# Kernel tuning notes

Measured on AMD Instinct MI355X. Metric: run time of the kernel, lower is better.

## Reference

```python
import jax, jax.numpy as jnp
import numpy as np

N, E, F_IN, F_E, H, T = 100000, 1600000, 128, 16, 64, 32
NEG_SLOPE = 0.2


def setup_inputs() -> dict:
    key = jax.random.key(0)
    ks = jax.random.split(key, 24)
    s = 0.1
    inp = {
        'x': jax.random.normal(ks[0], (N, F_IN), jnp.float32),
        'edge_index': jax.random.randint(ks[1], (2, E), 0, N, dtype=jnp.int32),
        'edge_attr': jax.random.normal(ks[2], (E, F_E), jnp.float32),
        # GATConv layer 1 (heads=1)
        'W1': jax.random.normal(ks[3], (F_IN, H), jnp.float32) * s,
        'as1': jax.random.normal(ks[4], (H,), jnp.float32) * s,
        'ad1': jax.random.normal(ks[5], (H,), jnp.float32) * s,
        'We1': jax.random.normal(ks[6], (F_E, H), jnp.float32) * s,
        'ae1': jax.random.normal(ks[7], (H,), jnp.float32) * s,
        'b1': jnp.zeros((H,), jnp.float32),
        # GATConv layer 2
        'W2': jax.random.normal(ks[8], (H, H), jnp.float32) * s,
        'as2': jax.random.normal(ks[9], (H,), jnp.float32) * s,
        'ad2': jax.random.normal(ks[10], (H,), jnp.float32) * s,
        'We2': jax.random.normal(ks[11], (F_E, H), jnp.float32) * s,
        'ae2': jax.random.normal(ks[12], (H,), jnp.float32) * s,
        'b2': jnp.zeros((H,), jnp.float32),
        # classifier MLP (dropout in eval mode -> identity)
        'Wc1': jax.random.normal(ks[13], (H, H // 2), jnp.float32) * s,
        'bc1': jnp.zeros((H // 2,), jnp.float32),
        'Wc2': jax.random.normal(ks[14], (H // 2, T), jnp.float32) * s,
        'bc2': jnp.zeros((T,), jnp.float32),
    }
    return inp


def gat_conv(x, src, dst, edge_attr, W, a_s, a_d, We, a_e, b):
    """Single-head PyG-style GATConv with edge features and self-loops
    (self-loop edge_attr = mean of incoming edge_attr, fill_value='mean')."""
    n = x.shape[0]
    # self loops with mean incoming edge features
    deg = jax.ops.segment_sum(jnp.ones_like(dst, jnp.float32), dst, n)
    loop_attr = jax.ops.segment_sum(edge_attr, dst, n) / jnp.maximum(deg, 1.0)[:, None]
    loops = jnp.arange(n, dtype=src.dtype)
    src_f = jnp.concatenate([src, loops])
    dst_f = jnp.concatenate([dst, loops])
    ea = jnp.concatenate([edge_attr, loop_attr], axis=0)  # [E+N, F_E]
    h = x @ W                                             # [N, H]
    # attention logits per edge: alpha_src[j] + alpha_dst[i] + alpha_edge
    alpha = (h @ a_s)[src_f] + (h @ a_d)[dst_f] + (ea @ We) @ a_e
    alpha = jax.nn.leaky_relu(alpha, NEG_SLOPE)
    # segment softmax over incoming edges per destination node
    m = jax.ops.segment_max(alpha, dst_f, n)
    p = jnp.exp(alpha - m[dst_f])
    z = jax.ops.segment_sum(p, dst_f, n)
    w = p / z[dst_f]                                      # [E+N]
    out = jax.ops.segment_sum(w[:, None] * h[src_f], dst_f, n)
    return out + b


def reference(x, edge_index, edge_attr, W1, as1, ad1, We1, ae1, b1,
              W2, as2, ad2, We2, ae2, b2, Wc1, bc1, Wc2, bc2):
    src, dst = edge_index[0], edge_index[1]
    h = jax.nn.relu(gat_conv(x, src, dst, edge_attr, W1, as1, ad1, We1, ae1, b1))
    h = jax.nn.relu(gat_conv(h, src, dst, edge_attr, W2, as2, ad2, We2, ae2, b2))
    h = jax.nn.relu(h @ Wc1 + bc1)
    logits = h @ Wc2 + bc2
    return logits
```

## Files before the change

kernel.cpp:

```cpp
#include <hip/hip_runtime.h>
#include <hip/hip_bf16.h>
#include <hip/hip_fp16.h>

#define NEG_SLOPE 0.2f
#define EPB 2048
#define NBUK 512

__device__ __forceinline__ float leaky(float a) { return a > 0.f ? a : NEG_SLOPE * a; }

__global__ __launch_bounds__(256) void count_pack(
    const int* __restrict__ dst, const float* __restrict__ eattr,
    const float* __restrict__ We1, const float* __restrict__ ae1,
    const float* __restrict__ We2, const float* __restrict__ ae2,
    unsigned int* __restrict__ meta_pay, int* __restrict__ counts, int E) {
    __shared__ float wvs[32];
    __shared__ int hist[NBUK];
    int tid = threadIdx.x, i = blockIdx.x;
    if (tid < 32) {
        const float* Wp = (tid < 16) ? We1 : We2;
        const float* ap = (tid < 16) ? ae1 : ae2;
        int f = tid & 15;
        float s = 0.f;
        for (int k = 0; k < 64; ++k) s += Wp[f * 64 + k] * ap[k];
        wvs[tid] = s;
    }
    for (int t = tid; t < NBUK; t += 256) hist[t] = 0;
    __syncthreads();
    int e0 = i * EPB, e1 = min(E, e0 + EPB);
    for (int e = e0 + tid; e < e1; e += 256) {
        int d = dst[e];
        atomicAdd(&hist[d >> 8], 1);
        const float4* ep = (const float4*)(eattr + (size_t)e * 16);
        float4 q0 = ep[0], q1 = ep[1], q2 = ep[2], q3 = ep[3];
        float a[16] = {q0.x, q0.y, q0.z, q0.w, q1.x, q1.y, q1.z, q1.w,
                       q2.x, q2.y, q2.z, q2.w, q3.x, q3.y, q3.z, q3.w};
        float s1 = 0.f, s2 = 0.f;
#pragma unroll
        for (int f = 0; f < 16; ++f) { s1 += a[f] * wvs[f]; s2 += a[f] * wvs[16 + f]; }
        unsigned int p1 = (unsigned int)__half_as_ushort(__float2half_rn(s1));
        unsigned int p2 = (unsigned int)__half_as_ushort(__float2half_rn(s2));
        meta_pay[e] = p1 | (p2 << 16);
    }
    __syncthreads();
    for (int t = tid; t < NBUK; t += 256) counts[(size_t)i * NBUK + t] = hist[t];
}

__global__ __launch_bounds__(1024) void scan_cols(const int* __restrict__ counts,
                                                  int* __restrict__ offsets,
                                                  int* __restrict__ btot, int nblk) {
    __shared__ int sh[1024];
    int b = blockIdx.x, t = threadIdx.x;
    int v = (t < nblk) ? counts[(size_t)t * NBUK + b] : 0;
    sh[t] = v;
    __syncthreads();
    for (int off = 1; off < 1024; off <<= 1) {
        int u = (t >= off) ? sh[t - off] : 0;
        __syncthreads();
        sh[t] += u;
        __syncthreads();
    }
    if (t < nblk) offsets[(size_t)t * NBUK + b] = sh[t] - v;
    if (t == 1023) btot[b] = sh[1023];
}

__global__ void scan_buckets(const int* __restrict__ btot, int* __restrict__ bbase,
                             int* __restrict__ rowptr, int E, int n) {
    __shared__ int sh[NBUK];
    int t = threadIdx.x;
    int v = btot[t];
    sh[t] = v;
    __syncthreads();
    for (int off = 1; off < NBUK; off <<= 1) {
        int u = (t >= off) ? sh[t - off] : 0;
        __syncthreads();
        sh[t] += u;
        __syncthreads();
    }
    bbase[t] = sh[t] - v;
    if (t == 0) rowptr[n] = E;
}

__global__ __launch_bounds__(256) void scatter_buckets(
    const int* __restrict__ dst, const int* __restrict__ src,
    const unsigned int* __restrict__ meta_pay, const int* __restrict__ offsets,
    const int* __restrict__ bbase, uint2* __restrict__ bucketed, int E) {
    __shared__ int cur[NBUK];
    int i = blockIdx.x, tid = threadIdx.x;
    for (int t = tid; t < NBUK; t += 256) cur[t] = bbase[t] + offsets[(size_t)i * NBUK + t];
    __syncthreads();
    int e0 = i * EPB, e1 = min(E, e0 + EPB);
    for (int e = e0 + tid; e < e1; e += 256) {
        int d = dst[e];
        int slot = atomicAdd(&cur[d >> 8], 1);
        bucketed[slot] = make_uint2((unsigned int)src[e] | ((unsigned int)(d & 255) << 24),
                                    meta_pay[e]);
    }
}

__global__ __launch_bounds__(256) void csr_build(const uint2* __restrict__ bucketed,
                                                 const int* __restrict__ bbase,
                                                 const int* __restrict__ btot,
                                                 int* __restrict__ rowptr,
                                                 uint2* __restrict__ recs, int n) {
    __shared__ int deg[256], sc[256], cur[256];
    int b = blockIdx.x, tid = threadIdx.x;
    int base = bbase[b], cnt = btot[b];
    deg[tid] = 0;
    __syncthreads();
    for (int k = tid; k < cnt; k += 256) {
        uint2 r = bucketed[base + k];
        atomicAdd(&deg[r.x >> 24], 1);
    }
    __syncthreads();
    int dv = deg[tid];
    sc[tid] = dv;
    __syncthreads();
    for (int off = 1; off < 256; off <<= 1) {
        int u = (tid >= off) ? sc[tid - off] : 0;
        __syncthreads();
        sc[tid] += u;
        __syncthreads();
    }
    int excl = sc[tid] - dv;
    int d = b * 256 + tid;
    if (d < n) rowptr[d] = base + excl;
    cur[tid] = base + excl;
    __syncthreads();
    for (int k = tid; k < cnt; k += 256) {
        uint2 r = bucketed[base + k];
        int dl = (int)(r.x >> 24);
        int pos = atomicAdd(&cur[dl], 1);
        recs[pos] = make_uint2(r.x & 0x00FFFFFFu, r.y);
    }
}

template <int K>
__global__ __launch_bounds__(256) void gemm_node(const float* __restrict__ X,
                                                 const float* __restrict__ W,
                                                 const float* __restrict__ a_s,
                                                 const float* __restrict__ a_d,
                                                 __half* __restrict__ Hout16,
                                                 float* __restrict__ ash,
                                                 float* __restrict__ adh, int n) {
    constexpr int KC = 64;
    __shared__ float xs[128 * 65];
    __shared__ float ws[KC * 64];
    int tid = threadIdx.x;
    int base = blockIdx.x * 128;
    int ct = tid & 7;
    int rt = tid >> 3;

    float acc[4][8];
#pragma unroll
    for (int i = 0; i < 4; ++i)
#pragma unroll
        for (int j = 0; j < 8; ++j) acc[i][j] = 0.f;

    for (int kc = 0; kc < K; kc += KC) {
#pragma unroll
        for (int p = 0; p < 8; ++p) {
            int idx = p * 256 + tid;
            int row = idx >> 4;
            int f4 = idx & 15;
            float4 q = make_float4(0.f, 0.f, 0.f, 0.f);
            if (base + row < n) q = *(const float4*)(X + (size_t)(base + row) * K + kc + f4 * 4);
            float* dp = xs + row * 65 + f4 * 4;
            dp[0] = q.x; dp[1] = q.y; dp[2] = q.z; dp[3] = q.w;
        }
#pragma unroll
        for (int p = 0; p < 4; ++p) {
            int idx = p * 256 + tid;
            int f = idx >> 4;
            int c4 = idx & 15;
            *(float4*)(ws + f * 64 + c4 * 4) =
                *(const float4*)(W + (size_t)(kc + f) * 64 + c4 * 4);
        }
        __syncthreads();
#pragma unroll 4
        for (int f = 0; f < KC; ++f) {
            float4 w0 = *(const float4*)(ws + f * 64 + ct * 8);
            float4 w1 = *(const float4*)(ws + f * 64 + ct * 8 + 4);
            float b0[8] = {w0.x, w0.y, w0.z, w0.w, w1.x, w1.y, w1.z, w1.w};
#pragma unroll
            for (int i = 0; i < 4; ++i) {
                float a = xs[(rt * 4 + i) * 65 + f];
#pragma unroll
                for (int j = 0; j < 8; ++j) acc[i][j] = fmaf(a, b0[j], acc[i][j]);
            }
        }
        __syncthreads();
    }

    float as_r[8], ad_r[8];
#pragma unroll
    for (int j = 0; j < 8; ++j) { as_r[j] = a_s[ct * 8 + j]; ad_r[j] = a_d[ct * 8 + j]; }
#pragma unroll
    for (int i = 0; i < 4; ++i) {
        int r = base + rt * 4 + i;
        float ps = 0.f, pd = 0.f;
#pragma unroll
        for (int j = 0; j < 8; ++j) {
            ps = fmaf(acc[i][j], as_r[j], ps);
            pd = fmaf(acc[i][j], ad_r[j], pd);
        }
        ps += __shfl_xor(ps, 1); pd += __shfl_xor(pd, 1);
        ps += __shfl_xor(ps, 2); pd += __shfl_xor(pd, 2);
        ps += __shfl_xor(ps, 4); pd += __shfl_xor(pd, 4);
        if (r < n) {
            union { __half h[8]; uint4 u; } pk;
#pragma unroll
            for (int j = 0; j < 8; ++j) pk.h[j] = __float2half_rn(acc[i][j]);
            *(uint4*)(Hout16 + (size_t)r * 64 + ct * 8) = pk.u;
            if (ct == 0) { ash[r] = ps; adh[r] = pd; }
        }
    }
}

template <int LAYER>
__global__ __launch_bounds__(256) void gat_aggregate(
    const __half* __restrict__ Hf, const float* __restrict__ ash, const float* __restrict__ adh,
    const int* __restrict__ rowptr, const uint2* __restrict__ recs,
    const float* __restrict__ bias, float* __restrict__ outp, int n) {
    int wave = threadIdx.x >> 6;
    int lane = threadIdx.x & 63;
    int i = blockIdx.x * 4 + wave;
    if (i >= n) return;
    int start = rowptr[i], end = rowptr[i + 1];
    float adi = adh[i];
    const char* Hb = (const char*)Hf;

    float acc = 0.f;
    float zl = 0.f, seal = 0.f;

    for (int c = start; c < end; c += 64) {
        int cnt = min(64, end - c);
        int o_l = 0;
        float p_l = 0.f;
        if (lane < cnt) {
            uint2 r = recs[c + lane];
            int s_l = (int)r.x;
            o_l = s_l << 7;
            unsigned short u = (LAYER == 0) ? (unsigned short)(r.y & 0xffffu)
                                            : (unsigned short)(r.y >> 16);
            float e = __half2float(__ushort_as_half(u));
            float p = __expf(leaky(ash[s_l] + adi + e));
            p_l = p;
            zl += p;
            seal += e;
        }
        int k = 0;
        for (; k + 4 <= cnt; k += 4) {
            int o0 = __builtin_amdgcn_readlane(o_l, k);
            int o1 = __builtin_amdgcn_readlane(o_l, k + 1);
            int o2 = __builtin_amdgcn_readlane(o_l, k + 2);
            int o3 = __builtin_amdgcn_readlane(o_l, k + 3);
            float p0 = __uint_as_float(__builtin_amdgcn_readlane((int)__float_as_uint(p_l), k));
            float p1 = __uint_as_float(__builtin_amdgcn_readlane((int)__float_as_uint(p_l), k + 1));
            float p2 = __uint_as_float(__builtin_amdgcn_readlane((int)__float_as_uint(p_l), k + 2));
            float p3 = __uint_as_float(__builtin_amdgcn_readlane((int)__float_as_uint(p_l), k + 3));
            float v0 = __half2float(((const __half*)(Hb + o0))[lane]);
            float v1 = __half2float(((const __half*)(Hb + o1))[lane]);
            float v2 = __half2float(((const __half*)(Hb + o2))[lane]);
            float v3 = __half2float(((const __half*)(Hb + o3))[lane]);
            acc = fmaf(p0, v0, acc);
            acc = fmaf(p1, v1, acc);
            acc = fmaf(p2, v2, acc);
            acc = fmaf(p3, v3, acc);
        }
        for (; k < cnt; ++k) {
            int o0 = __builtin_amdgcn_readlane(o_l, k);
            float p0 = __uint_as_float(__builtin_amdgcn_readlane((int)__float_as_uint(p_l), k));
            float v0 = __half2float(((const __half*)(Hb + o0))[lane]);
            acc = fmaf(p0, v0, acc);
        }
    }

    float z = zl, sea = seal;
#pragma unroll
    for (int off = 1; off < 64; off <<= 1) {
        z += __shfl_xor(z, off);
        sea += __shfl_xor(sea, off);
    }

    int d = end - start;
    float loop_sc = sea / (float)max(d, 1);
    float aself = leaky(ash[i] + adi + loop_sc);
    float pself = __expf(aself);
    z += pself;
    acc = fmaf(pself, __half2float(Hf[(size_t)i * 64 + lane]), acc);
    float o = acc / z + bias[lane];
    outp[(size_t)i * 64 + lane] = fmaxf(o, 0.f);
}

__global__ __launch_bounds__(256) void mlp_kernel(const float* __restrict__ X,
                                                  const float* __restrict__ Wc1,
                                                  const float* __restrict__ bc1,
                                                  const float* __restrict__ Wc2,
                                                  const float* __restrict__ bc2,
                                                  float* __restrict__ outp, int n) {
    __shared__ float v[8 * 64];
    __shared__ float tb[8 * 32];
    int base = blockIdx.x * 8;
    for (int t = threadIdx.x; t < 512; t += 256) {
        int r = t >> 6;
        v[t] = (base + r < n) ? X[(size_t)base * 64 + t] : 0.f;
    }
    __syncthreads();
    int r = threadIdx.x >> 5, j = threadIdx.x & 31;
    float acc = bc1[j];
#pragma unroll
    for (int k = 0; k < 64; ++k) acc += v[r * 64 + k] * Wc1[k * 32 + j];
    acc = fmaxf(acc, 0.f);
    tb[r * 32 + j] = acc;
    __syncthreads();
    float lg = bc2[j];
#pragma unroll
    for (int k2 = 0; k2 < 32; ++k2) lg += tb[r * 32 + k2] * Wc2[k2 * 32 + j];
    int row = base + r;
    if (row < n) outp[(size_t)row * 32 + j] = lg;
}

extern "C" void kernel_launch(void* const* d_in, const int* in_sizes, int n_in,
                              void* d_out, int out_size, void* d_ws, size_t ws_size,
                              hipStream_t stream) {
    const float* x    = (const float*)d_in[0];
    const int*   ei   = (const int*)d_in[1];
    const float* eatt = (const float*)d_in[2];
    const float* W1   = (const float*)d_in[3];
    const float* as1  = (const float*)d_in[4];
    const float* ad1  = (const float*)d_in[5];
    const float* We1  = (const float*)d_in[6];
    const float* ae1  = (const float*)d_in[7];
    const float* b1   = (const float*)d_in[8];
    const float* W2   = (const float*)d_in[9];
    const float* as2  = (const float*)d_in[10];
    const float* ad2  = (const float*)d_in[11];
    const float* We2  = (const float*)d_in[12];
    const float* ae2  = (const float*)d_in[13];
    const float* b2   = (const float*)d_in[14];
    const float* Wc1  = (const float*)d_in[15];
    const float* bc1  = (const float*)d_in[16];
    const float* Wc2  = (const float*)d_in[17];
    const float* bc2  = (const float*)d_in[18];

    int n = in_sizes[0] / 128;
    int E = in_sizes[1] / 2;
    const int* src = ei;
    const int* dst = ei + E;
    int nblk = (E + EPB - 1) / EPB;

    char* w = (char*)d_ws;
    auto alloc = [&](size_t bytes) { void* p = (void*)w; w += (bytes + 255) & ~(size_t)255; return p; };
    int* rowptr   = (int*)alloc((size_t)(n + 1) * 4);
    int* counts   = (int*)alloc((size_t)nblk * NBUK * 4);
    int* offsets  = (int*)alloc((size_t)nblk * NBUK * 4);
    int* btot     = (int*)alloc((size_t)NBUK * 4);
    int* bbase    = (int*)alloc((size_t)NBUK * 4);
    unsigned int* meta_pay = (unsigned int*)alloc((size_t)E * 4);
    uint2* recs   = (uint2*)alloc((size_t)E * 8);
    __half* hbuf16 = (__half*)alloc((size_t)n * 64 * 2);
    float* obuf   = (float*)alloc((size_t)n * 64 * 4);
    float* ash    = (float*)alloc((size_t)n * 4);
    float* adh    = (float*)alloc((size_t)n * 4);
    uint2* bucketed = (uint2*)obuf;

    count_pack<<<nblk, 256, 0, stream>>>(dst, eatt, We1, ae1, We2, ae2, meta_pay, counts, E);
    scan_cols<<<NBUK, 1024, 0, stream>>>(counts, offsets, btot, nblk);
    scan_buckets<<<1, NBUK, 0, stream>>>(btot, bbase, rowptr, E, n);
    scatter_buckets<<<nblk, 256, 0, stream>>>(dst, src, meta_pay, offsets, bbase, bucketed, E);
    csr_build<<<NBUK, 256, 0, stream>>>(bucketed, bbase, btot, rowptr, recs, n);

    gemm_node<128><<<(n + 127) / 128, 256, 0, stream>>>(x, W1, as1, ad1, hbuf16, ash, adh, n);
    gat_aggregate<0><<<(n + 3) / 4, 256, 0, stream>>>(hbuf16, ash, adh, rowptr, recs, b1, obuf, n);
    gemm_node<64><<<(n + 127) / 128, 256, 0, stream>>>(obuf, W2, as2, ad2, hbuf16, ash, adh, n);
    gat_aggregate<1><<<(n + 3) / 4, 256, 0, stream>>>(hbuf16, ash, adh, rowptr, recs, b2, obuf, n);
    mlp_kernel<<<(n + 7) / 8, 256, 0, stream>>>(obuf, Wc1, bc1, Wc2, bc2, (float*)d_out, n);
}
```

Before: 485.9 us.

## Gather four neighbours per wave step with 8-byte loads via LDS staging

```diff
diff --git a/kernel.cpp b/kernel.cpp
--- a/kernel.cpp
+++ b/kernel.cpp
@@ -221,6 +221,7 @@
     const __half* __restrict__ Hf, const float* __restrict__ ash, const float* __restrict__ adh,
     const int* __restrict__ rowptr, const uint2* __restrict__ recs,
     const float* __restrict__ bias, float* __restrict__ outp, int n) {
+    __shared__ uint2 ops[4][64];
     int wave = threadIdx.x >> 6;
     int lane = threadIdx.x & 63;
     int i = blockIdx.x * 4 + wave;
@@ -228,18 +229,20 @@
     int start = rowptr[i], end = rowptr[i + 1];
     float adi = adh[i];
     const char* Hb = (const char*)Hf;
-
-    float acc = 0.f;
+    int g = lane >> 4;
+    unsigned int fb = (unsigned int)((lane & 15) * 8);
+
+    float acc0 = 0.f, acc1 = 0.f, acc2 = 0.f, acc3 = 0.f;
     float zl = 0.f, seal = 0.f;
 
     for (int c = start; c < end; c += 64) {
         int cnt = min(64, end - c);
-        int o_l = 0;
+        unsigned int o_l = 0;
         float p_l = 0.f;
         if (lane < cnt) {
             uint2 r = recs[c + lane];
             int s_l = (int)r.x;
-            o_l = s_l << 7;
+            o_l = (unsigned int)s_l << 7;
             unsigned short u = (LAYER == 0) ? (unsigned short)(r.y & 0xffffu)
                                             : (unsigned short)(r.y >> 16);
             float e = __half2float(__ushort_as_half(u));
@@ -248,32 +251,26 @@
             zl += p;
             seal += e;
         }
-        int k = 0;
-        for (; k + 4 <= cnt; k += 4) {
-            int o0 = __builtin_amdgcn_readlane(o_l, k);
-            int o1 = __builtin_amdgcn_readlane(o_l, k + 1);
-            int o2 = __builtin_amdgcn_readlane(o_l, k + 2);
-            int o3 = __builtin_amdgcn_readlane(o_l, k + 3);
-            float p0 = __uint_as_float(__builtin_amdgcn_readlane((int)__float_as_uint(p_l), k));
-            float p1 = __uint_as_float(__builtin_amdgcn_readlane((int)__float_as_uint(p_l), k + 1));
-            float p2 = __uint_as_float(__builtin_amdgcn_readlane((int)__float_as_uint(p_l), k + 2));
-            float p3 = __uint_as_float(__builtin_amdgcn_readlane((int)__float_as_uint(p_l), k + 3));
-            float v0 = __half2float(((const __half*)(Hb + o0))[lane]);
-            float v1 = __half2float(((const __half*)(Hb + o1))[lane]);
-            float v2 = __half2float(((const __half*)(Hb + o2))[lane]);
-            float v3 = __half2float(((const __half*)(Hb + o3))[lane]);
-            acc = fmaf(p0, v0, acc);
-            acc = fmaf(p1, v1, acc);
-            acc = fmaf(p2, v2, acc);
-            acc = fmaf(p3, v3, acc);
-        }
-        for (; k < cnt; ++k) {
-            int o0 = __builtin_amdgcn_readlane(o_l, k);
-            float p0 = __uint_as_float(__builtin_amdgcn_readlane((int)__float_as_uint(p_l), k));
-            float v0 = __half2float(((const __half*)(Hb + o0))[lane]);
-            acc = fmaf(p0, v0, acc);
-        }
-    }
+        ops[wave][lane] = make_uint2(o_l, __float_as_uint(p_l));
+        int nq = (cnt + 3) >> 2;
+#pragma unroll 4
+        for (int q = 0; q < nq; ++q) {
+            uint2 op = ops[wave][q * 4 + g];
+            uint2 hv = *(const uint2*)(Hb + (op.x + fb));
+            float p = __uint_as_float(op.y);
+            __half2 h01 = *(__half2*)&hv.x;
+            __half2 h23 = *(__half2*)&hv.y;
+            acc0 = fmaf(p, __half2float(h01.x), acc0);
+            acc1 = fmaf(p, __half2float(h01.y), acc1);
+            acc2 = fmaf(p, __half2float(h23.x), acc2);
+            acc3 = fmaf(p, __half2float(h23.y), acc3);
+        }
+    }
+
+    acc0 += __shfl_xor(acc0, 16); acc1 += __shfl_xor(acc1, 16);
+    acc2 += __shfl_xor(acc2, 16); acc3 += __shfl_xor(acc3, 16);
+    acc0 += __shfl_xor(acc0, 32); acc1 += __shfl_xor(acc1, 32);
+    acc2 += __shfl_xor(acc2, 32); acc3 += __shfl_xor(acc3, 32);
 
     float z = zl, sea = seal;
 #pragma unroll
@@ -287,9 +284,24 @@
     float aself = leaky(ash[i] + adi + loop_sc);
     float pself = __expf(aself);
     z += pself;
-    acc = fmaf(pself, __half2float(Hf[(size_t)i * 64 + lane]), acc);
-    float o = acc / z + bias[lane];
-    outp[(size_t)i * 64 + lane] = fmaxf(o, 0.f);
+
+    uint2 hvs = *(const uint2*)(Hb + (((size_t)i << 7) + fb));
+    __half2 s01 = *(__half2*)&hvs.x;
+    __half2 s23 = *(__half2*)&hvs.y;
+    acc0 = fmaf(pself, __half2float(s01.x), acc0);
+    acc1 = fmaf(pself, __half2float(s01.y), acc1);
+    acc2 = fmaf(pself, __half2float(s23.x), acc2);
+    acc3 = fmaf(pself, __half2float(s23.y), acc3);
+
+    if (lane < 16) {
+        float4 bv = *(const float4*)(bias + lane * 4);
+        float4 o;
+        o.x = fmaxf(acc0 / z + bv.x, 0.f);
+        o.y = fmaxf(acc1 / z + bv.y, 0.f);
+        o.z = fmaxf(acc2 / z + bv.z, 0.f);
+        o.w = fmaxf(acc3 / z + bv.w, 0.f);
+        *(float4*)(outp + (size_t)i * 64 + lane * 4) = o;
+    }
 }
 
 __global__ __launch_bounds__(256) void mlp_kernel(const float* __restrict__ X,
```

New measurement: 477.5 us. About the same (-1.7%).
